# Performance work log

Hardware: AMD Instinct MI355X
Metric: run time of the kernel (lower is better)

## Reference

```python
import jax, jax.numpy as jnp
import numpy as np

B, D, T, K = 16, 512, 4096, 1024

def setup_inputs() -> dict:
    key = jax.random.key(0)
    kx, kc = jax.random.split(key)
    x = jax.random.normal(kx, (B, D, T), dtype=jnp.float32)
    codebook = jax.random.normal(kc, (K, D), dtype=jnp.float32)
    return {"x": x, "codebook": codebook}

def reference(x, codebook):
    # x: [B, D, T] -> xt: [B, T, D]
    xt = jnp.transpose(x, (0, 2, 1))
    x_sq = jnp.sum(xt * xt, axis=-1, keepdims=True)          # [B, T, 1]
    c_sq = jnp.sum(codebook * codebook, axis=-1)             # [K]
    cross = jnp.einsum('btd,kd->btk', xt, codebook)          # [B, T, K]
    dist = x_sq - 2.0 * cross + c_sq                         # [B, T, K]
    indexes = jnp.argmin(dist, axis=2)                       # [B, T] int
    quantized = codebook[indexes]                            # [B, T, D]
    quantized = jnp.transpose(quantized, (0, 2, 1))          # [B, D, T]
    return quantized, indexes
```

## Files before the change

### kernel.cpp

```cpp
#include <hip/hip_runtime.h>

#define BB 16
#define DD 512
#define TT 4096
#define KK 1024

typedef _Float16 h16;
typedef __attribute__((ext_vector_type(8))) _Float16 half8;
typedef __attribute__((ext_vector_type(4))) float float4v;

#define XTH_OFF 0ull
#define XTL_OFF 67108864ull
#define CBH_OFF 134217728ull
#define CBL_OFF 135266304ull
#define CSQ_OFF 136314880ull
#define WS_NEED (136314880ull + 4096ull)

#define GLOAD_LDS16(g, l) __builtin_amdgcn_global_load_lds( \
    (const __attribute__((address_space(1))) void*)(g),      \
    (__attribute__((address_space(3))) void*)(l), 16, 0, 0)

__global__ void csq_kernel(const float* __restrict__ cb, float* __restrict__ csq) {
    int wave = threadIdx.x >> 6;
    int lane = threadIdx.x & 63;
    int row  = blockIdx.x * 4 + wave;
    const float* r = cb + (size_t)row * DD;
    float s = 0.f;
    #pragma unroll
    for (int i = 0; i < DD / 64; ++i) { float v = r[lane + i * 64]; s += v * v; }
    #pragma unroll
    for (int off = 32; off; off >>= 1) s += __shfl_down(s, off, 64);
    if (lane == 0) csq[row] = s;
}

__global__ __launch_bounds__(256) void split_x_kernel(const float* __restrict__ x,
                                                      h16* __restrict__ xth,
                                                      h16* __restrict__ xtl) {
    __shared__ float xs[64][68];
    const int b = blockIdx.z, d0 = blockIdx.y * 64, t0 = blockIdx.x * 64;
    const int tid = threadIdx.x;
    const float* xp = x + ((size_t)b * DD + d0) * TT + t0;
    #pragma unroll
    for (int j = 0; j < 4; ++j) {
        int i4 = tid + 256 * j;
        int dd = i4 >> 4, tp = (i4 & 15) << 2;
        float4 v = *(const float4*)(xp + (size_t)dd * TT + tp);
        *(float4*)&xs[dd][tp] = v;
    }
    __syncthreads();
    const int tt = tid & 63, dq = (tid >> 6) << 4;
    h16 hv[16], lv[16];
    #pragma unroll
    for (int i = 0; i < 16; ++i) {
        float v = xs[dq + i][tt];
        h16 h = (h16)v;
        hv[i] = h;
        lv[i] = (h16)(v - (float)h);
    }
    size_t o = ((size_t)b * TT + t0 + tt) * DD + d0 + dq;
    *(half8*)(xth + o)     = *(half8*)&hv[0];
    *(half8*)(xth + o + 8) = *(half8*)&hv[8];
    *(half8*)(xtl + o)     = *(half8*)&lv[0];
    *(half8*)(xtl + o + 8) = *(half8*)&lv[8];
}

__global__ void split_cb_kernel(const float* __restrict__ cb,
                                h16* __restrict__ cbh, h16* __restrict__ cbl) {
    int g = blockIdx.x * 256 + threadIdx.x;
    float4 v = *(const float4*)(cb + (size_t)g * 4);
    h16 h[4], l[4];
    float vv[4] = {v.x, v.y, v.z, v.w};
    #pragma unroll
    for (int i = 0; i < 4; ++i) {
        h[i] = (h16)vv[i];
        l[i] = (h16)(vv[i] - (float)h[i]);
    }
    *(ushort4*)(cbh + (size_t)g * 4) = *(ushort4*)h;
    *(ushort4*)(cbl + (size_t)g * 4) = *(ushort4*)l;
}

__global__ __launch_bounds__(256, 2) void mfma_argmin_kernel(
    const h16* __restrict__ xth, const h16* __restrict__ xtl,
    const h16* __restrict__ cbh, const h16* __restrict__ cbl,
    const float* __restrict__ csq, float* __restrict__ idx_f_out) {

    __shared__ h16 ash[128 * 64];
    __shared__ h16 asl[128 * 64];
    __shared__ h16 bsh[128 * 64];
    __shared__ h16 bsl[128 * 64];
    __shared__ float redv[2][128];
    __shared__ int   redi[2][128];

    const int tid = threadIdx.x;
    const int wid = tid >> 6, lane = tid & 63;
    const int wm = wid & 1, wn = wid >> 1;
    const int b = blockIdx.y, t0 = blockIdx.x * 128;
    const int lr = lane >> 3;
    const int lc = (lane & 7) * 8;
    const int c  = lane & 15;
    const int q  = lane >> 4;

    const h16* xhb = xth + ((size_t)b * TT + t0) * DD;
    const h16* xlb = xtl + ((size_t)b * TT + t0) * DD;

    float best[16];
    int   bidx[16];
    #pragma unroll
    for (int i = 0; i < 16; ++i) { best[i] = 3.4e38f; bidx[i] = 0; }

    for (int kc = 0; kc < KK; kc += 128) {
        float4v acc[4][4];
        #pragma unroll
        for (int m = 0; m < 4; ++m)
            #pragma unroll
            for (int n = 0; n < 4; ++n)
                acc[m][n] = (float4v){0.f, 0.f, 0.f, 0.f};

        for (int dc = 0; dc < DD; dc += 64) {
            __syncthreads();
            const int rbase = wid * 32;
            #pragma unroll
            for (int i = 0; i < 4; ++i) {
                int r = rbase + i * 8;
                GLOAD_LDS16(xhb + (size_t)(r + lr) * DD + dc + lc, ash + r * 64);
                GLOAD_LDS16(xlb + (size_t)(r + lr) * DD + dc + lc, asl + r * 64);
                GLOAD_LDS16(cbh + (size_t)(kc + r + lr) * DD + dc + lc, bsh + r * 64);
                GLOAD_LDS16(cbl + (size_t)(kc + r + lr) * DD + dc + lc, bsl + r * 64);
            }
            __syncthreads();

            #pragma unroll
            for (int ks = 0; ks < 2; ++ks) {
                const int doff = ks * 32 + q * 8;
                half8 Ah[4], Al[4];
                #pragma unroll
                for (int m = 0; m < 4; ++m) {
                    int row = wm * 64 + m * 16 + c;
                    Ah[m] = *(const half8*)(ash + row * 64 + doff);
                    Al[m] = *(const half8*)(asl + row * 64 + doff);
                }
                #pragma unroll
                for (int n = 0; n < 4; ++n) {
                    int row = wn * 64 + n * 16 + c;
                    half8 Bh = *(const half8*)(bsh + row * 64 + doff);
                    half8 Bl = *(const half8*)(bsl + row * 64 + doff);
                    #pragma unroll
                    for (int m = 0; m < 4; ++m) {
                        acc[m][n] = __builtin_amdgcn_mfma_f32_16x16x32_f16(Ah[m], Bh, acc[m][n], 0, 0, 0);
                        acc[m][n] = __builtin_amdgcn_mfma_f32_16x16x32_f16(Ah[m], Bl, acc[m][n], 0, 0, 0);
                        acc[m][n] = __builtin_amdgcn_mfma_f32_16x16x32_f16(Al[m], Bh, acc[m][n], 0, 0, 0);
                    }
                }
            }
        }
        #pragma unroll
        for (int n = 0; n < 4; ++n) {
            int kg = kc + wn * 64 + n * 16 + c;
            float cq = csq[kg];
            #pragma unroll
            for (int m = 0; m < 4; ++m)
                #pragma unroll
                for (int r = 0; r < 4; ++r) {
                    float s = fmaf(-2.0f, acc[m][n][r], cq);
                    int slot = m * 4 + r;
                    if (s < best[slot]) { best[slot] = s; bidx[slot] = kg; }
                }
        }
    }

    #pragma unroll
    for (int slot = 0; slot < 16; ++slot) {
        float v = best[slot]; int i = bidx[slot];
        #pragma unroll
        for (int d = 1; d < 16; d <<= 1) {
            float pv = __shfl_xor(v, d);
            int   pi = __shfl_xor(i, d);
            if (pv < v || (pv == v && pi < i)) { v = pv; i = pi; }
        }
        if (c == 0) {
            int m = slot >> 2, r = slot & 3;
            int tl = wm * 64 + m * 16 + q * 4 + r;
            redv[wn][tl] = v; redi[wn][tl] = i;
        }
    }
    __syncthreads();
    if (tid < 128) {
        float v0 = redv[0][tid]; int i0 = redi[0][tid];
        float v1 = redv[1][tid]; int i1 = redi[1][tid];
        if (v1 < v0 || (v1 == v0 && i1 < i0)) { v0 = v1; i0 = i1; }
        idx_f_out[(size_t)b * TT + t0 + tid] = (float)i0;
    }
}

__global__ void gather_kernel(const float* __restrict__ cb,
                              const float* __restrict__ idx_f,
                              float* __restrict__ out) {
    int b  = blockIdx.y;
    int t  = blockIdx.x * 256 + threadIdx.x;
    int d0 = blockIdx.z * (DD / 4);
    int k  = (int)idx_f[(size_t)b * TT + t];
    const float* row = cb + (size_t)k * DD;
    float* ob = out + (size_t)b * DD * TT + t;
    #pragma unroll 8
    for (int d = d0; d < d0 + DD / 4; ++d)
        ob[(size_t)d * TT] = row[d];
}

__global__ __launch_bounds__(256) void argmin_fp32_kernel(
    const float* __restrict__ x, const float* __restrict__ cb,
    const float* __restrict__ csq, float* __restrict__ idx_f_out) {

    __shared__ float xs[32][128];
    __shared__ float cs[32][132];

    const int tid = threadIdx.x;
    const int b = blockIdx.y;
    const int t_blk = blockIdx.x * 128;
    const int tq = tid & 15, kq = tid >> 4;
    const int t0 = tq * 8, k0 = kq * 8;
    const float* xb = x + (size_t)b * DD * TT;

    float best[8]; int bidx[8];
    #pragma unroll
    for (int i = 0; i < 8; ++i) { best[i] = 3.4e38f; bidx[i] = 0; }

    for (int kc = 0; kc < KK; kc += 128) {
        float acc[8][8];
        #pragma unroll
        for (int i = 0; i < 8; ++i)
            #pragma unroll
            for (int j = 0; j < 8; ++j) acc[i][j] = 0.f;
        for (int dc = 0; dc < DD; dc += 32) {
            __syncthreads();
            #pragma unroll
            for (int j = 0; j < 4; ++j) {
                int i4 = tid + 256 * j;
                int dd = i4 >> 5, tp = (i4 & 31) << 2;
                *(float4*)&xs[dd][tp] =
                    *(const float4*)(xb + (size_t)(dc + dd) * TT + t_blk + tp);
            }
            #pragma unroll
            for (int j = 0; j < 4; ++j) {
                int i4 = tid + 256 * j;
                int kk = i4 >> 3, dq = (i4 & 7) << 2;
                float4 v = *(const float4*)(cb + (size_t)(kc + kk) * DD + dc + dq);
                cs[dq + 0][kk] = v.x; cs[dq + 1][kk] = v.y;
                cs[dq + 2][kk] = v.z; cs[dq + 3][kk] = v.w;
            }
            __syncthreads();
            #pragma unroll 8
            for (int dd = 0; dd < 32; ++dd) {
                float a[8], bv[8];
                *(float4*)&a[0]  = *(const float4*)&xs[dd][t0];
                *(float4*)&a[4]  = *(const float4*)&xs[dd][t0 + 4];
                *(float4*)&bv[0] = *(const float4*)&cs[dd][k0];
                *(float4*)&bv[4] = *(const float4*)&cs[dd][k0 + 4];
                #pragma unroll
                for (int i = 0; i < 8; ++i)
                    #pragma unroll
                    for (int j = 0; j < 8; ++j)
                        acc[i][j] = fmaf(a[i], bv[j], acc[i][j]);
            }
        }
        #pragma unroll
        for (int j = 0; j < 8; ++j) {
            int kg = kc + k0 + j;
            float cq = csq[kg];
            #pragma unroll
            for (int i = 0; i < 8; ++i) {
                float s = cq - 2.0f * acc[i][j];
                if (s < best[i]) { best[i] = s; bidx[i] = kg; }
            }
        }
    }
    __syncthreads();
    float* rbest = &xs[0][0];
    int*   ridx  = (int*)&cs[0][0];
    #pragma unroll
    for (int i = 0; i < 8; ++i) {
        rbest[kq * 128 + t0 + i] = best[i];
        ridx [kq * 128 + t0 + i] = bidx[i];
    }
    __syncthreads();
    if (tid < 128) {
        float bv = rbest[tid]; int bi = ridx[tid];
        #pragma unroll
        for (int g = 1; g < 16; ++g) {
            float v = rbest[g * 128 + tid]; int ii = ridx[g * 128 + tid];
            if (v < bv || (v == bv && ii < bi)) { bv = v; bi = ii; }
        }
        idx_f_out[(size_t)b * TT + t_blk + tid] = (float)bi;
    }
}

extern "C" void kernel_launch(void* const* d_in, const int* in_sizes, int n_in,
                              void* d_out, int out_size, void* d_ws, size_t ws_size,
                              hipStream_t stream) {
    const float* x  = (const float*)d_in[0];
    const float* cb = (const float*)d_in[1];
    float* out   = (float*)d_out;
    float* idx_f = out + (size_t)BB * DD * TT;

    if (ws_size >= WS_NEED) {
        h16* xth = (h16*)((char*)d_ws + XTH_OFF);
        h16* xtl = (h16*)((char*)d_ws + XTL_OFF);
        h16* cbh = (h16*)((char*)d_ws + CBH_OFF);
        h16* cbl = (h16*)((char*)d_ws + CBL_OFF);
        float* csq = (float*)((char*)d_ws + CSQ_OFF);

        csq_kernel<<<KK / 4, 256, 0, stream>>>(cb, csq);
        split_cb_kernel<<<(KK * DD / 4) / 256, 256, 0, stream>>>(cb, cbh, cbl);
        split_x_kernel<<<dim3(TT / 64, DD / 64, BB), 256, 0, stream>>>(x, xth, xtl);
        mfma_argmin_kernel<<<dim3(TT / 128, BB), 256, 0, stream>>>(
            xth, xtl, cbh, cbl, csq, idx_f);
        gather_kernel<<<dim3(TT / 256, BB, 4), 256, 0, stream>>>(cb, idx_f, out);
    } else {
        float* csq = (float*)d_ws;
        csq_kernel<<<KK / 4, 256, 0, stream>>>(cb, csq);
        argmin_fp32_kernel<<<dim3(TT / 128, BB), 256, 0, stream>>>(x, cb, csq, idx_f);
        gather_kernel<<<dim3(TT / 256, BB, 4), 256, 0, stream>>>(cb, idx_f, out);
    }
}
```

Before: 510.8 us.

## Pre-tile split fp16 operands into contiguous blocks and fuse gather into argmin

The split kernels now write x and codebook hi/lo halves in a blocked layout of 128-row by 32-column tiles stored contiguously, so each K-step of the MFMA kernel loads whole tiles with linear global-to-LDS copies. The D-step shrinks from 64 to 32 and LDS use halves, and launch bounds allow three blocks per CU. The gather into the transposed output is fused into the argmin kernel's epilogue, which removes a separate launch and the index round-trip. The costs are twice as many barriers per D-sweep and a gather that now runs inside the compute kernel's tail.

```diff
diff --git a/kernel.cpp b/kernel.cpp
--- a/kernel.cpp
+++ b/kernel.cpp
@@ -36,79 +36,92 @@
 __global__ __launch_bounds__(256) void split_x_kernel(const float* __restrict__ x,
                                                       h16* __restrict__ xth,
                                                       h16* __restrict__ xtl) {
-    __shared__ float xs[64][68];
-    const int b = blockIdx.z, d0 = blockIdx.y * 64, t0 = blockIdx.x * 64;
+    __shared__ float xs[32][132];
+    const int tb = blockIdx.x, dcb = blockIdx.y, b = blockIdx.z;
     const int tid = threadIdx.x;
+    const int t0 = tb * 128, d0 = dcb * 32;
     const float* xp = x + ((size_t)b * DD + d0) * TT + t0;
     #pragma unroll
     for (int j = 0; j < 4; ++j) {
         int i4 = tid + 256 * j;
-        int dd = i4 >> 4, tp = (i4 & 15) << 2;
-        float4 v = *(const float4*)(xp + (size_t)dd * TT + tp);
-        *(float4*)&xs[dd][tp] = v;
-    }
-    __syncthreads();
-    const int tt = tid & 63, dq = (tid >> 6) << 4;
+        int dd = i4 >> 5, c4 = (i4 & 31) << 2;
+        *(float4*)&xs[dd][c4] = *(const float4*)(xp + (size_t)dd * TT + c4);
+    }
+    __syncthreads();
+    const int r = tid >> 1;
+    const int ch = (tid & 1) * 16;
     h16 hv[16], lv[16];
     #pragma unroll
     for (int i = 0; i < 16; ++i) {
-        float v = xs[dq + i][tt];
+        float v = xs[ch + i][r];
         h16 h = (h16)v;
         hv[i] = h;
         lv[i] = (h16)(v - (float)h);
     }
-    size_t o = ((size_t)b * TT + t0 + tt) * DD + d0 + dq;
+    size_t o = (((size_t)(b * 32 + tb) * 16) + dcb) * 4096 + (size_t)tid * 16;
     *(half8*)(xth + o)     = *(half8*)&hv[0];
     *(half8*)(xth + o + 8) = *(half8*)&hv[8];
     *(half8*)(xtl + o)     = *(half8*)&lv[0];
     *(half8*)(xtl + o + 8) = *(half8*)&lv[8];
 }
 
-__global__ void split_cb_kernel(const float* __restrict__ cb,
-                                h16* __restrict__ cbh, h16* __restrict__ cbl) {
-    int g = blockIdx.x * 256 + threadIdx.x;
-    float4 v = *(const float4*)(cb + (size_t)g * 4);
-    h16 h[4], l[4];
-    float vv[4] = {v.x, v.y, v.z, v.w};
-    #pragma unroll
-    for (int i = 0; i < 4; ++i) {
-        h[i] = (h16)vv[i];
-        l[i] = (h16)(vv[i] - (float)h[i]);
-    }
-    *(ushort4*)(cbh + (size_t)g * 4) = *(ushort4*)h;
-    *(ushort4*)(cbl + (size_t)g * 4) = *(ushort4*)l;
-}
-
-__global__ __launch_bounds__(256, 2) void mfma_argmin_kernel(
+__global__ __launch_bounds__(256) void split_cb_kernel(const float* __restrict__ cb,
+                                                       h16* __restrict__ cbh,
+                                                       h16* __restrict__ cbl) {
+    const int kb = blockIdx.x >> 4, dcb = blockIdx.x & 15;
+    const int tid = threadIdx.x;
+    const float* cp = cb + ((size_t)kb * 128) * DD + dcb * 32;
+    h16* oh = cbh + ((size_t)(kb * 16 + dcb)) * 4096;
+    h16* ol = cbl + ((size_t)(kb * 16 + dcb)) * 4096;
+    #pragma unroll
+    for (int j = 0; j < 4; ++j) {
+        int i4 = tid + 256 * j;
+        int rr = i4 >> 3, c4 = (i4 & 7) << 2;
+        float4 v = *(const float4*)(cp + (size_t)rr * DD + c4);
+        float vv[4] = {v.x, v.y, v.z, v.w};
+        h16 h[4], l[4];
+        #pragma unroll
+        for (int i = 0; i < 4; ++i) {
+            h[i] = (h16)vv[i];
+            l[i] = (h16)(vv[i] - (float)h[i]);
+        }
+        *(ushort4*)(oh + rr * 32 + c4) = *(ushort4*)h;
+        *(ushort4*)(ol + rr * 32 + c4) = *(ushort4*)l;
+    }
+}
+
+__global__ __launch_bounds__(256, 3) void mfma_argmin_kernel(
     const h16* __restrict__ xth, const h16* __restrict__ xtl,
     const h16* __restrict__ cbh, const h16* __restrict__ cbl,
-    const float* __restrict__ csq, float* __restrict__ idx_f_out) {
-
-    __shared__ h16 ash[128 * 64];
-    __shared__ h16 asl[128 * 64];
-    __shared__ h16 bsh[128 * 64];
-    __shared__ h16 bsl[128 * 64];
+    const float* __restrict__ csq, const float* __restrict__ cb,
+    float* __restrict__ idx_f_out, float* __restrict__ out) {
+
+    __shared__ h16 ash[4096];
+    __shared__ h16 asl[4096];
+    __shared__ h16 bsh[4096];
+    __shared__ h16 bsl[4096];
     __shared__ float redv[2][128];
     __shared__ int   redi[2][128];
 
     const int tid = threadIdx.x;
     const int wid = tid >> 6, lane = tid & 63;
     const int wm = wid & 1, wn = wid >> 1;
-    const int b = blockIdx.y, t0 = blockIdx.x * 128;
-    const int lr = lane >> 3;
-    const int lc = (lane & 7) * 8;
+    const int tb = blockIdx.x, b = blockIdx.y;
+    const int t0 = tb * 128;
     const int c  = lane & 15;
     const int q  = lane >> 4;
 
-    const h16* xhb = xth + ((size_t)b * TT + t0) * DD;
-    const h16* xlb = xtl + ((size_t)b * TT + t0) * DD;
+    const h16* aH = xth + ((size_t)(b * 32 + tb) * 16) * 4096;
+    const h16* aL = xtl + ((size_t)(b * 32 + tb) * 16) * 4096;
 
     float best[16];
     int   bidx[16];
     #pragma unroll
     for (int i = 0; i < 16; ++i) { best[i] = 3.4e38f; bidx[i] = 0; }
 
-    for (int kc = 0; kc < KK; kc += 128) {
+    for (int kci = 0; kci < 8; ++kci) {
+        const h16* bH = cbh + (size_t)kci * 16 * 4096;
+        const h16* bL = cbl + (size_t)kci * 16 * 4096;
         float4v acc[4][4];
         #pragma unroll
         for (int m = 0; m < 4; ++m)
@@ -116,46 +129,42 @@
             for (int n = 0; n < 4; ++n)
                 acc[m][n] = (float4v){0.f, 0.f, 0.f, 0.f};
 
-        for (int dc = 0; dc < DD; dc += 64) {
+        for (int dcb = 0; dcb < 16; ++dcb) {
             __syncthreads();
-            const int rbase = wid * 32;
-            #pragma unroll
-            for (int i = 0; i < 4; ++i) {
-                int r = rbase + i * 8;
-                GLOAD_LDS16(xhb + (size_t)(r + lr) * DD + dc + lc, ash + r * 64);
-                GLOAD_LDS16(xlb + (size_t)(r + lr) * DD + dc + lc, asl + r * 64);
-                GLOAD_LDS16(cbh + (size_t)(kc + r + lr) * DD + dc + lc, bsh + r * 64);
-                GLOAD_LDS16(cbl + (size_t)(kc + r + lr) * DD + dc + lc, bsl + r * 64);
+            #pragma unroll
+            for (int j = 0; j < 2; ++j) {
+                int off = (tid + 256 * j) * 8;
+                GLOAD_LDS16(aH + (size_t)dcb * 4096 + off, ash + off);
+                GLOAD_LDS16(aL + (size_t)dcb * 4096 + off, asl + off);
+                GLOAD_LDS16(bH + (size_t)dcb * 4096 + off, bsh + off);
+                GLOAD_LDS16(bL + (size_t)dcb * 4096 + off, bsl + off);
             }
             __syncthreads();
 
-            #pragma unroll
-            for (int ks = 0; ks < 2; ++ks) {
-                const int doff = ks * 32 + q * 8;
-                half8 Ah[4], Al[4];
+            const int doff = q * 8;
+            half8 Ah[4], Al[4];
+            #pragma unroll
+            for (int m = 0; m < 4; ++m) {
+                int row = wm * 64 + m * 16 + c;
+                Ah[m] = *(const half8*)(ash + row * 32 + doff);
+                Al[m] = *(const half8*)(asl + row * 32 + doff);
+            }
+            #pragma unroll
+            for (int n = 0; n < 4; ++n) {
+                int row = wn * 64 + n * 16 + c;
+                half8 Bh = *(const half8*)(bsh + row * 32 + doff);
+                half8 Bl = *(const half8*)(bsl + row * 32 + doff);
                 #pragma unroll
                 for (int m = 0; m < 4; ++m) {
-                    int row = wm * 64 + m * 16 + c;
-                    Ah[m] = *(const half8*)(ash + row * 64 + doff);
-                    Al[m] = *(const half8*)(asl + row * 64 + doff);
+                    acc[m][n] = __builtin_amdgcn_mfma_f32_16x16x32_f16(Ah[m], Bh, acc[m][n], 0, 0, 0);
+                    acc[m][n] = __builtin_amdgcn_mfma_f32_16x16x32_f16(Ah[m], Bl, acc[m][n], 0, 0, 0);
+                    acc[m][n] = __builtin_amdgcn_mfma_f32_16x16x32_f16(Al[m], Bh, acc[m][n], 0, 0, 0);
                 }
-                #pragma unroll
-                for (int n = 0; n < 4; ++n) {
-                    int row = wn * 64 + n * 16 + c;
-                    half8 Bh = *(const half8*)(bsh + row * 64 + doff);
-                    half8 Bl = *(const half8*)(bsl + row * 64 + doff);
-                    #pragma unroll
-                    for (int m = 0; m < 4; ++m) {
-                        acc[m][n] = __builtin_amdgcn_mfma_f32_16x16x32_f16(Ah[m], Bh, acc[m][n], 0, 0, 0);
-                        acc[m][n] = __builtin_amdgcn_mfma_f32_16x16x32_f16(Ah[m], Bl, acc[m][n], 0, 0, 0);
-                        acc[m][n] = __builtin_amdgcn_mfma_f32_16x16x32_f16(Al[m], Bh, acc[m][n], 0, 0, 0);
-                    }
-                }
             }
         }
         #pragma unroll
         for (int n = 0; n < 4; ++n) {
-            int kg = kc + wn * 64 + n * 16 + c;
+            int kg = kci * 128 + wn * 64 + n * 16 + c;
             float cq = csq[kg];
             #pragma unroll
             for (int m = 0; m < 4; ++m)
@@ -189,6 +198,21 @@
         float v1 = redv[1][tid]; int i1 = redi[1][tid];
         if (v1 < v0 || (v1 == v0 && i1 < i0)) { v0 = v1; i0 = i1; }
         idx_f_out[(size_t)b * TT + t0 + tid] = (float)i0;
+        redi[0][tid] = i0;
+    }
+    __syncthreads();
+
+    const int tl = tid & 127, dg = tid >> 7;
+    const int k = redi[0][tl];
+    const float* row = cb + (size_t)k * DD + dg * 256;
+    float* ob = out + ((size_t)b * DD + dg * 256) * TT + t0 + tl;
+    #pragma unroll 4
+    for (int i = 0; i < 64; ++i) {
+        float4 v = *(const float4*)(row + i * 4);
+        ob[(size_t)(i * 4 + 0) * TT] = v.x;
+        ob[(size_t)(i * 4 + 1) * TT] = v.y;
+        ob[(size_t)(i * 4 + 2) * TT] = v.z;
+        ob[(size_t)(i * 4 + 3) * TT] = v.w;
     }
 }
 
@@ -309,11 +333,10 @@
         float* csq = (float*)((char*)d_ws + CSQ_OFF);
 
         csq_kernel<<<KK / 4, 256, 0, stream>>>(cb, csq);
-        split_cb_kernel<<<(KK * DD / 4) / 256, 256, 0, stream>>>(cb, cbh, cbl);
-        split_x_kernel<<<dim3(TT / 64, DD / 64, BB), 256, 0, stream>>>(x, xth, xtl);
+        split_cb_kernel<<<128, 256, 0, stream>>>(cb, cbh, cbl);
+        split_x_kernel<<<dim3(TT / 128, DD / 32, BB), 256, 0, stream>>>(x, xth, xtl);
         mfma_argmin_kernel<<<dim3(TT / 128, BB), 256, 0, stream>>>(
-            xth, xtl, cbh, cbl, csq, idx_f);
-        gather_kernel<<<dim3(TT / 256, BB, 4), 256, 0, stream>>>(cb, idx_f, out);
+            xth, xtl, cbh, cbl, csq, cb, idx_f, out);
     } else {
         float* csq = (float*)d_ws;
         csq_kernel<<<KK / 4, 256, 0, stream>>>(cb, csq);
```

After: 486.3 us. -4.8%, faster.
